# Optimization experiments

Hardware: AMD Instinct MI355X
Metric: run time of the kernel (lower is better)

The kernel has to match this reference:

```python
import jax, jax.numpy as jnp
import numpy as np
from jax.scipy.linalg import expm

N_MODES, N_LAYERS, CUTOFF, BATCH = 6, 6, 3, 1024
M2 = N_MODES * (N_MODES - 1) // 2                  # beamsplitter thetas per interferometer
N_IF = N_MODES * (N_MODES - 1) + (N_MODES - 1)     # interferometer param count = 35

_np_a = np.diag(np.sqrt(np.arange(1, CUTOFF)), 1)  # truncated annihilation operator
A = jnp.asarray(_np_a, jnp.complex64)
AD = A.conj().T
NVEC = jnp.arange(CUTOFF, dtype=jnp.float32)       # number operator diagonal
X_OP = A + AD                                      # x quadrature (hbar=2, PennyLane/SF convention)
BS_GEN = jnp.kron(AD, A) - jnp.kron(A, AD)         # Beamsplitter(theta, 0) generator
SQ_GEN = A @ A - AD @ AD                           # Squeezing(r, 0) generator (times r/2)
D_GEN = AD - A                                     # Displacement(r, 0) generator

def disp_gate(r):
    return expm(r.astype(jnp.complex64) * D_GEN)

def sq_gate(r):
    return expm(0.5 * r.astype(jnp.complex64) * SQ_GEN)

def bs_gate(theta):
    return expm(theta.astype(jnp.complex64) * BS_GEN)

def apply_1(psi, U, m):
    # psi: (B, D, ..., D); apply DxD gate U on mode m
    psi = jnp.moveaxis(psi, 1 + m, -1)
    psi = psi @ U.T
    return jnp.moveaxis(psi, -1, 1 + m)

def apply_1_batched(psi, U, m):
    # U: (B, D, D) per-sample gate (data-encoding displacement)
    psi = jnp.moveaxis(psi, 1 + m, -1)
    psi = jnp.einsum('b...j,bij->b...i', psi, U)
    return jnp.moveaxis(psi, -1, 1 + m)

def apply_2(psi, U, m):
    psi = jnp.moveaxis(psi, (1 + m, 2 + m), (-2, -1))
    sh = psi.shape
    psi = (psi.reshape(sh[:-2] + (CUTOFF * CUTOFF,)) @ U.T).reshape(sh)
    return jnp.moveaxis(psi, (-2, -1), (1 + m, 2 + m))

def apply_diag(psi, d, m):
    shape = [1] * psi.ndim
    shape[1 + m] = CUTOFF
    return psi * d.reshape(shape)

def interferometer(psi, params):
    theta = params[:M2]
    rphi = params[-N_MODES:]  # faithful to source: overlaps last (unused) phi param
    n = 0
    for l in range(N_MODES):
        for k in range(N_MODES - 1):
            if (l + k) % 2 != 1:
                psi = apply_2(psi, bs_gate(theta[n]), k)
                n += 1
    for i in range(max(1, N_MODES - 1)):
        psi = apply_diag(psi, jnp.exp(1j * rphi[i] * NVEC), i)
    return psi

def cv_forward(x, theta_1, theta_2, squeezing_r, displacement_r, kerr_params):
    B = x.shape[0]
    psi = jnp.zeros((B,) + (CUTOFF,) * N_MODES, jnp.complex64)
    psi = psi.at[(slice(None),) + (0,) * N_MODES].set(1.0)  # |0...0> vacuum
    for m in range(N_MODES):  # data-encoding displacements, per-sample gates
        psi = apply_1_batched(psi, jax.vmap(disp_gate)(x[:, m]), m)
    for L in range(N_LAYERS):
        psi = interferometer(psi, theta_1[L])
        for m in range(N_MODES):
            psi = apply_1(psi, sq_gate(squeezing_r[L, m] * 0.5), m)
        psi = interferometer(psi, theta_2[L])
        for m in range(N_MODES):
            psi = apply_1(psi, disp_gate(displacement_r[L, m]), m)
            psi = apply_diag(psi, jnp.exp(1j * (kerr_params[L, m] * 0.001) * NVEC * NVEC), m)
    sum_axes = tuple(range(1, psi.ndim))
    outs = [jnp.sum(jnp.conj(psi) * apply_1(psi, X_OP, m), axis=sum_axes).real
            for m in range(N_MODES)]
    return jnp.stack(outs, axis=1)  # (B, N_MODES)

def setup_inputs() -> dict:
    key = jax.random.key(0)
    ks = jax.random.split(key, 6)
    passive_sd = 0.01 * np.pi
    return {
        'x': jax.random.normal(ks[0], (BATCH, N_MODES), jnp.float32),
        'theta_1': jax.random.normal(ks[1], (N_LAYERS, N_IF), jnp.float32) * passive_sd,
        'theta_2': jax.random.normal(ks[2], (N_LAYERS, N_IF), jnp.float32) * np.float32(0.2 * np.pi),
        'squeezing_r': jax.random.normal(ks[3], (N_LAYERS, N_MODES), jnp.float32) * 1e-3,
        'displacement_r': jax.random.normal(ks[4], (N_LAYERS, N_MODES), jnp.float32) * 1e-3,
        'kerr_params': jax.random.normal(ks[5], (N_LAYERS, N_MODES), jnp.float32) * 1e-3,
    }

def reference(x, theta_1, theta_2, squeezing_r, displacement_r, kerr_params):
    return cv_forward(x, theta_1, theta_2, squeezing_r, displacement_r, kerr_params)
```

## Files before the change

### kernel.cpp

```cpp
#include <hip/hip_runtime.h>

#define SQRT2f 1.41421356237309515f
#define SQRT3f 1.73205080756887729f

__device__ __forceinline__ float2 cmul(float2 a, float2 b) {
  return make_float2(a.x*b.x - a.y*b.y, a.x*b.y + a.y*b.x);
}
__device__ __forceinline__ float2 cadd(float2 a, float2 b) {
  return make_float2(a.x + b.x, a.y + b.y);
}

__device__ __forceinline__ void bs_q(float2 q[9], float2 cs) {
  const float c = cs.x, s = cs.y;
  const float c2 = c*c - s*s, s2 = 2.f*c*s;
  const float cc = c*c, ss = s*s, rcs = SQRT2f*c*s;
  float2 a1=q[1], a3=q[3], a2=q[2], a4=q[4], a6=q[6], a5=q[5], a7=q[7];
  q[1] = make_float2(c*a1.x - s*a3.x, c*a1.y - s*a3.y);
  q[3] = make_float2(s*a1.x + c*a3.x, s*a1.y + c*a3.y);
  q[2] = make_float2(cc*a2.x - rcs*a4.x + ss*a6.x, cc*a2.y - rcs*a4.y + ss*a6.y);
  q[4] = make_float2(rcs*a2.x + c2*a4.x - rcs*a6.x, rcs*a2.y + c2*a4.y - rcs*a6.y);
  q[6] = make_float2(ss*a2.x + rcs*a4.x + cc*a6.x, ss*a2.y + rcs*a4.y + cc*a6.y);
  q[5] = make_float2(c2*a5.x - s2*a7.x, c2*a5.y - s2*a7.y);
  q[7] = make_float2(s2*a5.x + c2*a7.x, s2*a5.y + c2*a7.y);
}

template<int SP>
__device__ __forceinline__ void bs_nonet(float2* __restrict__ psi, int base,
                                         float2 cs) {
  const float c = cs.x, s = cs.y;
  const float c2 = c*c - s*s, s2 = 2.f*c*s;
  const float cc = c*c, ss = s*s, rcs = SQRT2f*c*s;
  float2 a1 = psi[base+SP],   a3 = psi[base+3*SP];
  float2 a2 = psi[base+2*SP], a4 = psi[base+4*SP], a6 = psi[base+6*SP];
  float2 a5 = psi[base+5*SP], a7 = psi[base+7*SP];
  psi[base+SP]   = make_float2(c*a1.x - s*a3.x, c*a1.y - s*a3.y);
  psi[base+3*SP] = make_float2(s*a1.x + c*a3.x, s*a1.y + c*a3.y);
  psi[base+2*SP] = make_float2(cc*a2.x - rcs*a4.x + ss*a6.x,
                               cc*a2.y - rcs*a4.y + ss*a6.y);
  psi[base+4*SP] = make_float2(rcs*a2.x + c2*a4.x - rcs*a6.x,
                               rcs*a2.y + c2*a4.y - rcs*a6.y);
  psi[base+6*SP] = make_float2(ss*a2.x + rcs*a4.x + cc*a6.x,
                               ss*a2.y + rcs*a4.y + cc*a6.y);
  psi[base+5*SP] = make_float2(c2*a5.x - s2*a7.x, c2*a5.y - s2*a7.y);
  psi[base+7*SP] = make_float2(s2*a5.x + c2*a7.x, s2*a5.y + c2*a7.y);
}

template<int SP>
__device__ __forceinline__ void dpbs_nonet(float2* __restrict__ psi, int base,
                                           const float2* __restrict__ G,
                                           float2 cs) {
  const float2* A = G; const float2* B = G + 9;
  float2 v[3][3];
#pragma unroll
  for (int j = 0; j < 3; ++j)
#pragma unroll
    for (int jb = 0; jb < 3; ++jb) v[j][jb] = psi[base + j*3*SP + jb*SP];
  float2 t[3][3];
#pragma unroll
  for (int j = 0; j < 3; ++j)
#pragma unroll
    for (int ib = 0; ib < 3; ++ib)
      t[j][ib] = cadd(cadd(cmul(B[ib*3+0],v[j][0]), cmul(B[ib*3+1],v[j][1])),
                      cmul(B[ib*3+2],v[j][2]));
  float2 q[9];
#pragma unroll
  for (int i = 0; i < 3; ++i)
#pragma unroll
    for (int ib = 0; ib < 3; ++ib)
      q[i*3+ib] = cadd(cadd(cmul(A[i*3+0],t[0][ib]), cmul(A[i*3+1],t[1][ib])),
                       cmul(A[i*3+2],t[2][ib]));
  bs_q(q, cs);
#pragma unroll
  for (int i = 0; i < 3; ++i)
#pragma unroll
    for (int ib = 0; ib < 3; ++ib) psi[base + i*3*SP + ib*SP] = q[i*3+ib];
}

template<int SP>
__device__ __forceinline__ void sqbs_nonet(float2* __restrict__ psi, int base,
                                           const float2* __restrict__ G,
                                           float2 cs) {
  float2 A00=G[0],A02=G[1],A11=G[2],A20=G[3],A22=G[4];
  float2 B00=G[5],B02=G[6],B11=G[7],B20=G[8],B22=G[9];
  float2 v[3][3];
#pragma unroll
  for (int j = 0; j < 3; ++j)
#pragma unroll
    for (int jb = 0; jb < 3; ++jb) v[j][jb] = psi[base + j*3*SP + jb*SP];
  float2 t[3][3];
#pragma unroll
  for (int j = 0; j < 3; ++j) {
    t[j][0] = cadd(cmul(B00,v[j][0]), cmul(B02,v[j][2]));
    t[j][1] = cmul(B11,v[j][1]);
    t[j][2] = cadd(cmul(B20,v[j][0]), cmul(B22,v[j][2]));
  }
  float2 q[9];
#pragma unroll
  for (int ib = 0; ib < 3; ++ib) {
    q[ib]   = cadd(cmul(A00,t[0][ib]), cmul(A02,t[2][ib]));
    q[3+ib] = cmul(A11,t[1][ib]);
    q[6+ib] = cadd(cmul(A20,t[0][ib]), cmul(A22,t[2][ib]));
  }
  bs_q(q, cs);
#pragma unroll
  for (int i = 0; i < 3; ++i)
#pragma unroll
    for (int ib = 0; ib < 3; ++ib) psi[base + i*3*SP + ib*SP] = q[i*3+ib];
}

#define BASE4(g, s0,s1,s2,s3) ({ int _d=(g); int _b=(_d%3)*(s0); _d/=3; \
  _b += (_d%3)*(s1); _d/=3; _b += (_d%3)*(s2); _d/=3; _b += (_d%3)*(s3); _b; })
#define BASE5(g, s0,s1,s2,s3,s4) ({ int _d=(g); int _b=(_d%3)*(s0); _d/=3; \
  _b += (_d%3)*(s1); _d/=3; _b += (_d%3)*(s2); _d/=3; _b += (_d%3)*(s3); _d/=3; \
  _b += (_d%3)*(s4); _b; })

__device__ __forceinline__ float2 dpk_entry(const float* __restrict__ dr,
                                            const float* __restrict__ th2,
                                            const float* __restrict__ kp,
                                            int L, int mode, int i, int j) {
  float sn, cn; sincosf(SQRT3f*dr[L*6+mode], &sn, &cn);
  float sw = sn*(1.f/SQRT3f), cw = (1.f-cn)*(1.f/3.f);
  float U;
  if      (i==0) U = (j==0) ? (1.f-cw)     : (j==1) ? (-sw)         : (SQRT2f*cw);
  else if (i==1) U = (j==0) ? (sw)         : (j==1) ? (1.f-3.f*cw)  : (-SQRT2f*sw);
  else           U = (j==0) ? (SQRT2f*cw)  : (j==1) ? (SQRT2f*sw)   : (1.f-2.f*cw);
  float2 ph = make_float2(1.f, 0.f);
  if (mode < 5) { float ps, pc; sincosf(th2[L*35+29+mode], &ps, &pc);
                  ph = make_float2(pc, ps); }
  float2 phj = (j==0) ? make_float2(1.f,0.f) : (j==1) ? ph : cmul(ph, ph);
  float ks, kc; sincosf(0.001f*kp[L*6+mode], &ks, &kc);
  float2 k1 = make_float2(kc, ks);
  float2 ki = (i==0) ? make_float2(1.f,0.f)
            : (i==1) ? k1 : cmul(cmul(k1,k1), cmul(k1,k1));
  float2 t = cmul(phj, ki);
  return make_float2(U*t.x, U*t.y);
}

__global__ __launch_bounds__(128)
void cvnn_kernel(const float* __restrict__ x,
                 const float* __restrict__ th1,
                 const float* __restrict__ th2,
                 const float* __restrict__ sr,
                 const float* __restrict__ dr,
                 const float* __restrict__ kp,
                 float* __restrict__ out) {
  __shared__ float2 psi[729];
  __shared__ float2 gtab[690];
  __shared__ float red[12];

  const int tid = threadIdx.x;
  const int bidx = blockIdx.x;

  for (int f = tid; f < 690; f += 128) {
    float sn, cn; float2 v;
    if (f < 180) {
      int Lp = f/15, pos = f%15;
      int L = Lp/2, pass = Lp%2;
      float th = (pass ? th2 : th1)[L*35 + pos];
      sincosf(th, &sn, &cn); v = make_float2(cn, sn);
    } else if (f < 360) {
      int i = f - 180; int Lc = i/10, e = i%10;
      int L = Lc/3, c3 = Lc%3;
      int mode = 2*c3 + (e >= 5); int ee = e%5;
      float Sq, Cq; sincosf(0.25f*SQRT2f*sr[L*6+mode], &Sq, &Cq);
      float2 ph = make_float2(1.f, 0.f);
      if (mode < 5) { float ps, pc; sincosf(th1[L*35+29+mode], &ps, &pc);
                      ph = make_float2(pc, ps); }
      float2 ph2 = cmul(ph, ph);
      if      (ee == 0) v = make_float2(Cq, 0.f);
      else if (ee == 1) v = make_float2(Sq*ph2.x, Sq*ph2.y);
      else if (ee == 2) v = ph;
      else if (ee == 3) v = make_float2(-Sq, 0.f);
      else              v = make_float2(Cq*ph2.x, Cq*ph2.y);
    } else if (f < 630) {
      int i = f - 360; int Ld = i/18, e = i%18;
      int Ls = Ld/3, c3 = Ld%3;
      int mode = 2*c3 + (e >= 9); int ee = e%9;
      v = dpk_entry(dr, th2, kp, Ls, mode, ee/3, ee%3);
    } else if (f < 684) {
      int i = f - 630; int m = i/9, e = i%9;
      int ii = e/3, jj = e%3;
      float2 D0i = dpk_entry(dr, th2, kp, 5, m, 0, ii);
      float2 D1i = dpk_entry(dr, th2, kp, 5, m, 1, ii);
      float2 D2i = dpk_entry(dr, th2, kp, 5, m, 2, ii);
      float2 D0j = dpk_entry(dr, th2, kp, 5, m, 0, jj);
      float2 D1j = dpk_entry(dr, th2, kp, 5, m, 1, jj);
      float2 D2j = dpk_entry(dr, th2, kp, 5, m, 2, jj);
      float2 c0 = make_float2(D0i.x, -D0i.y);
      float2 c1 = make_float2(D1i.x, -D1i.y);
      float2 c2 = make_float2(D2i.x, -D2i.y);
      float2 acc = cmul(c0, D1j);
      float2 tmp = make_float2(D0j.x + SQRT2f*D2j.x, D0j.y + SQRT2f*D2j.y);
      acc = cadd(acc, cmul(c1, tmp));
      acc = cadd(acc, cmul(c2, make_float2(SQRT2f*D1j.x, SQRT2f*D1j.y)));
      v = acc;
    } else {
      int mode = f - 684;
      sincosf(SQRT3f*x[bidx*6 + mode], &sn, &cn);
      v = make_float2(sn*(1.f/SQRT3f), (1.f-cn)*(1.f/3.f));
    }
    gtab[f] = v;
  }
  __syncthreads();

  for (int idx = tid; idx < 729; idx += 128) {
    float pr = 1.f; int d = idx;
#pragma unroll
    for (int mm = 5; mm >= 0; --mm) {
      int n = d % 3; d /= 3;
      float2 dc = gtab[684 + mm];
      pr *= (n==0) ? (1.f-dc.y) : (n==1) ? dc.x : SQRT2f*dc.y;
    }
    psi[idx] = make_float2(pr, 0.f);
  }

  const bool act = (tid < 81);
  const int g = (tid < 81) ? tid : 0;
  const int b0 = g;
  const int b1 = BASE4(g, 1, 3, 9, 243);
  const int b2 = BASE4(g, 1, 3, 81, 243);
  const int b3 = BASE4(g, 1, 27, 81, 243);
  const int b4 = BASE4(g, 9, 27, 81, 243);
  __syncthreads();

  float2 csN = gtab[0];
  __syncthreads();

#define BSP(SP, BB, NEXT)  { if (act) bs_nonet<SP>(psi, BB, csN); \
    csN = gtab[NEXT]; __syncthreads(); }
#define DPBS(SP, BB, GI, NEXT) { if (act) dpbs_nonet<SP>(psi, BB, &gtab[GI], csN); \
    csN = gtab[NEXT]; __syncthreads(); }
#define SQBS(SP, BB, GI, NEXT) { if (act) sqbs_nonet<SP>(psi, BB, &gtab[GI], csN); \
    csN = gtab[NEXT]; __syncthreads(); }

#pragma unroll
  for (int L = 0; L < 6; ++L) {
    const int i1 = (L*2)*15, i2 = (L*2+1)*15;
    if (L == 0) {
      BSP(81, b0, i1+1); BSP(9, b2, i1+2); BSP(1, b4, i1+3);
    } else {
      const int gd = 360 + (L-1)*3*18;
      DPBS(81, b0, gd+0,  i1+1); DPBS(9, b2, gd+18, i1+2); DPBS(1, b4, gd+36, i1+3);
    }
    BSP(27, b1, i1+4);  BSP(3, b3, i1+5);
    BSP(81, b0, i1+6);  BSP(9, b2, i1+7);  BSP(1, b4, i1+8);
    BSP(27, b1, i1+9);  BSP(3, b3, i1+10);
    BSP(81, b0, i1+11); BSP(9, b2, i1+12); BSP(1, b4, i1+13);
    BSP(27, b1, i1+14); BSP(3, b3, i2+0);
    {
      const int gs = 180 + L*3*10;
      SQBS(81, b0, gs+0, i2+1); SQBS(9, b2, gs+10, i2+2); SQBS(1, b4, gs+20, i2+3);
    }
    BSP(27, b1, i2+4);  BSP(3, b3, i2+5);
    BSP(81, b0, i2+6);  BSP(9, b2, i2+7);  BSP(1, b4, i2+8);
    BSP(27, b1, i2+9);  BSP(3, b3, i2+10);
    BSP(81, b0, i2+11); BSP(9, b2, i2+12); BSP(1, b4, i2+13);
    BSP(27, b1, i2+14); BSP(3, b3, (L < 5) ? (L+1)*30 : 0);
  }

  float xs[6] = {0.f, 0.f, 0.f, 0.f, 0.f, 0.f};
  for (int it = 0; it < 2; ++it) {
    int t = tid + (it << 7);
    if (t < 243) {
#define XACC(m, SS, BB) { int b_ = (BB); \
      float2 a_ = psi[b_]; float2 e_ = psi[b_+(SS)]; float2 f_ = psi[b_+2*(SS)]; \
      const float2* M_ = &gtab[630 + (m)*9]; \
      float d0 = M_[0].x, d1 = M_[4].x, d2 = M_[8].x; \
      float2 M01 = M_[1], M02 = M_[2], M12 = M_[5]; \
      xs[m] += d0*(a_.x*a_.x + a_.y*a_.y) + d1*(e_.x*e_.x + e_.y*e_.y) \
             + d2*(f_.x*f_.x + f_.y*f_.y) \
        + 2.f*(M01.x*(a_.x*e_.x + a_.y*e_.y) - M01.y*(a_.x*e_.y - a_.y*e_.x)) \
        + 2.f*(M02.x*(a_.x*f_.x + a_.y*f_.y) - M02.y*(a_.x*f_.y - a_.y*f_.x)) \
        + 2.f*(M12.x*(e_.x*f_.x + e_.y*f_.y) - M12.y*(e_.x*f_.y - e_.y*f_.x)); }
      XACC(0, 243, BASE5(t, 1, 3, 9, 27, 81));
      XACC(1, 81,  BASE5(t, 1, 3, 9, 27, 243));
      XACC(2, 27,  BASE5(t, 1, 3, 9, 81, 243));
      XACC(3, 9,   BASE5(t, 1, 3, 27, 81, 243));
      XACC(4, 3,   BASE5(t, 1, 9, 27, 81, 243));
      XACC(5, 1,   BASE5(t, 3, 9, 27, 81, 243));
    }
  }
  const int lane = tid & 63, wid = tid >> 6;
#pragma unroll
  for (int m = 0; m < 6; ++m) {
    float v = xs[m];
    for (int off = 32; off > 0; off >>= 1) v += __shfl_down(v, off);
    if (lane == 0) red[wid*6 + m] = v;
  }
  __syncthreads();
  if (tid < 6) out[bidx*6 + tid] = red[tid] + red[6 + tid];
}

extern "C" void kernel_launch(void* const* d_in, const int* in_sizes, int n_in,
                              void* d_out, int out_size, void* d_ws, size_t ws_size,
                              hipStream_t stream) {
  const float* x  = (const float*)d_in[0];
  const float* t1 = (const float*)d_in[1];
  const float* t2 = (const float*)d_in[2];
  const float* sr = (const float*)d_in[3];
  const float* dr = (const float*)d_in[4];
  const float* kp = (const float*)d_in[5];
  const int B = in_sizes[0] / 6;
  cvnn_kernel<<<B, 128, 0, stream>>>(x, t1, t2, sr, dr, kp, (float*)d_out);
}
```

Baseline: 92.86 us.

## Pad last mode to 4 and process two-amplitude float4 groups per thread

```diff
diff --git a/kernel.cpp b/kernel.cpp
--- a/kernel.cpp
+++ b/kernel.cpp
@@ -10,102 +10,184 @@
   return make_float2(a.x + b.x, a.y + b.y);
 }
 
-__device__ __forceinline__ void bs_q(float2 q[9], float2 cs) {
-  const float c = cs.x, s = cs.y;
-  const float c2 = c*c - s*s, s2 = 2.f*c*s;
-  const float cc = c*c, ss = s*s, rcs = SQRT2f*c*s;
-  float2 a1=q[1], a3=q[3], a2=q[2], a4=q[4], a6=q[6], a5=q[5], a7=q[7];
-  q[1] = make_float2(c*a1.x - s*a3.x, c*a1.y - s*a3.y);
-  q[3] = make_float2(s*a1.x + c*a3.x, s*a1.y + c*a3.y);
-  q[2] = make_float2(cc*a2.x - rcs*a4.x + ss*a6.x, cc*a2.y - rcs*a4.y + ss*a6.y);
-  q[4] = make_float2(rcs*a2.x + c2*a4.x - rcs*a6.x, rcs*a2.y + c2*a4.y - rcs*a6.y);
-  q[6] = make_float2(ss*a2.x + rcs*a4.x + cc*a6.x, ss*a2.y + rcs*a4.y + cc*a6.y);
-  q[5] = make_float2(c2*a5.x - s2*a7.x, c2*a5.y - s2*a7.y);
-  q[7] = make_float2(s2*a5.x + c2*a7.x, s2*a5.y + c2*a7.y);
-}
-
-template<int SP>
-__device__ __forceinline__ void bs_nonet(float2* __restrict__ psi, int base,
-                                         float2 cs) {
-  const float c = cs.x, s = cs.y;
-  const float c2 = c*c - s*s, s2 = 2.f*c*s;
-  const float cc = c*c, ss = s*s, rcs = SQRT2f*c*s;
-  float2 a1 = psi[base+SP],   a3 = psi[base+3*SP];
-  float2 a2 = psi[base+2*SP], a4 = psi[base+4*SP], a6 = psi[base+6*SP];
-  float2 a5 = psi[base+5*SP], a7 = psi[base+7*SP];
-  psi[base+SP]   = make_float2(c*a1.x - s*a3.x, c*a1.y - s*a3.y);
-  psi[base+3*SP] = make_float2(s*a1.x + c*a3.x, s*a1.y + c*a3.y);
-  psi[base+2*SP] = make_float2(cc*a2.x - rcs*a4.x + ss*a6.x,
-                               cc*a2.y - rcs*a4.y + ss*a6.y);
-  psi[base+4*SP] = make_float2(rcs*a2.x + c2*a4.x - rcs*a6.x,
-                               rcs*a2.y + c2*a4.y - rcs*a6.y);
-  psi[base+6*SP] = make_float2(ss*a2.x + rcs*a4.x + cc*a6.x,
-                               ss*a2.y + rcs*a4.y + cc*a6.y);
-  psi[base+5*SP] = make_float2(c2*a5.x - s2*a7.x, c2*a5.y - s2*a7.y);
-  psi[base+7*SP] = make_float2(s2*a5.x + c2*a7.x, s2*a5.y + c2*a7.y);
-}
-
-template<int SP>
-__device__ __forceinline__ void dpbs_nonet(float2* __restrict__ psi, int base,
-                                           const float2* __restrict__ G,
-                                           float2 cs) {
-  const float2* A = G; const float2* B = G + 9;
-  float2 v[3][3];
-#pragma unroll
-  for (int j = 0; j < 3; ++j)
-#pragma unroll
-    for (int jb = 0; jb < 3; ++jb) v[j][jb] = psi[base + j*3*SP + jb*SP];
-  float2 t[3][3];
-#pragma unroll
-  for (int j = 0; j < 3; ++j)
-#pragma unroll
-    for (int ib = 0; ib < 3; ++ib)
-      t[j][ib] = cadd(cadd(cmul(B[ib*3+0],v[j][0]), cmul(B[ib*3+1],v[j][1])),
-                      cmul(B[ib*3+2],v[j][2]));
-  float2 q[9];
-#pragma unroll
-  for (int i = 0; i < 3; ++i)
-#pragma unroll
-    for (int ib = 0; ib < 3; ++ib)
-      q[i*3+ib] = cadd(cadd(cmul(A[i*3+0],t[0][ib]), cmul(A[i*3+1],t[1][ib])),
-                       cmul(A[i*3+2],t[2][ib]));
-  bs_q(q, cs);
-#pragma unroll
-  for (int i = 0; i < 3; ++i)
-#pragma unroll
-    for (int ib = 0; ib < 3; ++ib) psi[base + i*3*SP + ib*SP] = q[i*3+ib];
-}
-
-template<int SP>
-__device__ __forceinline__ void sqbs_nonet(float2* __restrict__ psi, int base,
-                                           const float2* __restrict__ G,
-                                           float2 cs) {
+__device__ __forceinline__ float4 f4m(float a, float4 v) {
+  return make_float4(a*v.x, a*v.y, a*v.z, a*v.w);
+}
+__device__ __forceinline__ float4 f4ma(float a, float4 v, float4 acc) {
+  return make_float4(acc.x+a*v.x, acc.y+a*v.y, acc.z+a*v.z, acc.w+a*v.w);
+}
+__device__ __forceinline__ float4 f4ms(float a, float4 v, float4 acc) {
+  return make_float4(acc.x-a*v.x, acc.y-a*v.y, acc.z-a*v.z, acc.w-a*v.w);
+}
+__device__ __forceinline__ float4 cmul4(float2 C, float4 v) {
+  return make_float4(C.x*v.x - C.y*v.y, C.x*v.y + C.y*v.x,
+                     C.x*v.z - C.y*v.w, C.x*v.w + C.y*v.z);
+}
+__device__ __forceinline__ float4 cfma4(float2 C, float4 v, float4 acc) {
+  return make_float4(acc.x + C.x*v.x - C.y*v.y, acc.y + C.x*v.y + C.y*v.x,
+                     acc.z + C.x*v.z - C.y*v.w, acc.w + C.x*v.w + C.y*v.z);
+}
+
+#define BS4C(v01,v02,v10,v11,v12,v20,v21, c,s,c2,s2,cc,ss,rcs) { \
+  { float4 t1=v01, t3=v10; \
+    v01 = f4ms(s,t3,f4m(c,t1)); v10 = f4ma(c,t3,f4m(s,t1)); } \
+  { float4 t2=v02, t4=v11, t6=v20; \
+    v02 = f4ma(ss,t6, f4ms(rcs,t4, f4m(cc,t2))); \
+    v11 = f4ms(rcs,t6, f4ma(c2,t4, f4m(rcs,t2))); \
+    v20 = f4ma(cc,t6, f4ma(rcs,t4, f4m(ss,t2))); } \
+  { float4 t5=v12, t7=v21; \
+    v12 = f4ms(s2,t7, f4m(c2,t5)); v21 = f4ma(c2,t7, f4m(s2,t5)); } }
+
+template<int SO, int SI>
+__device__ __forceinline__ void bs_w(float4* __restrict__ P, int b, float2 cs) {
+  const float c=cs.x, s=cs.y;
+  const float c2=c*c-s*s, s2=2.f*c*s, cc=c*c, ss=s*s, rcs=SQRT2f*c*s;
+  float4 v01=P[b+SI],      v10=P[b+SO];
+  float4 v02=P[b+2*SI],    v11=P[b+SO+SI],  v20=P[b+2*SO];
+  float4 v12=P[b+SO+2*SI], v21=P[b+2*SO+SI];
+  BS4C(v01,v02,v10,v11,v12,v20,v21, c,s,c2,s2,cc,ss,rcs);
+  P[b+SI]=v01; P[b+SO]=v10; P[b+2*SI]=v02; P[b+SO+SI]=v11; P[b+2*SO]=v20;
+  P[b+SO+2*SI]=v12; P[b+2*SO+SI]=v21;
+}
+
+template<int SO, int SI>
+__device__ __forceinline__ void sqbs_w(float4* __restrict__ P, int b,
+                                       const float2* __restrict__ G, float2 cs) {
   float2 A00=G[0],A02=G[1],A11=G[2],A20=G[3],A22=G[4];
   float2 B00=G[5],B02=G[6],B11=G[7],B20=G[8],B22=G[9];
-  float2 v[3][3];
-#pragma unroll
-  for (int j = 0; j < 3; ++j)
-#pragma unroll
-    for (int jb = 0; jb < 3; ++jb) v[j][jb] = psi[base + j*3*SP + jb*SP];
-  float2 t[3][3];
-#pragma unroll
-  for (int j = 0; j < 3; ++j) {
-    t[j][0] = cadd(cmul(B00,v[j][0]), cmul(B02,v[j][2]));
-    t[j][1] = cmul(B11,v[j][1]);
-    t[j][2] = cadd(cmul(B20,v[j][0]), cmul(B22,v[j][2]));
-  }
-  float2 q[9];
-#pragma unroll
-  for (int ib = 0; ib < 3; ++ib) {
-    q[ib]   = cadd(cmul(A00,t[0][ib]), cmul(A02,t[2][ib]));
-    q[3+ib] = cmul(A11,t[1][ib]);
-    q[6+ib] = cadd(cmul(A20,t[0][ib]), cmul(A22,t[2][ib]));
-  }
-  bs_q(q, cs);
-#pragma unroll
-  for (int i = 0; i < 3; ++i)
-#pragma unroll
-    for (int ib = 0; ib < 3; ++ib) psi[base + i*3*SP + ib*SP] = q[i*3+ib];
+  float4 v00=P[b],      v01=P[b+SI],      v02=P[b+2*SI];
+  float4 v10=P[b+SO],   v11=P[b+SO+SI],   v12=P[b+SO+2*SI];
+  float4 v20=P[b+2*SO], v21=P[b+2*SO+SI], v22=P[b+2*SO+2*SI];
+  { float4 u0=v00,u2=v02; v00=cfma4(B02,u2,cmul4(B00,u0)); v01=cmul4(B11,v01); v02=cfma4(B22,u2,cmul4(B20,u0)); }
+  { float4 u0=v10,u2=v12; v10=cfma4(B02,u2,cmul4(B00,u0)); v11=cmul4(B11,v11); v12=cfma4(B22,u2,cmul4(B20,u0)); }
+  { float4 u0=v20,u2=v22; v20=cfma4(B02,u2,cmul4(B00,u0)); v21=cmul4(B11,v21); v22=cfma4(B22,u2,cmul4(B20,u0)); }
+  { float4 u0=v00,u2=v20; v00=cfma4(A02,u2,cmul4(A00,u0)); v10=cmul4(A11,v10); v20=cfma4(A22,u2,cmul4(A20,u0)); }
+  { float4 u0=v01,u2=v21; v01=cfma4(A02,u2,cmul4(A00,u0)); v11=cmul4(A11,v11); v21=cfma4(A22,u2,cmul4(A20,u0)); }
+  { float4 u0=v02,u2=v22; v02=cfma4(A02,u2,cmul4(A00,u0)); v12=cmul4(A11,v12); v22=cfma4(A22,u2,cmul4(A20,u0)); }
+  const float c=cs.x, s=cs.y;
+  const float c2=c*c-s*s, s2=2.f*c*s, cc=c*c, ss=s*s, rcs=SQRT2f*c*s;
+  BS4C(v01,v02,v10,v11,v12,v20,v21, c,s,c2,s2,cc,ss,rcs);
+  P[b]=v00; P[b+SI]=v01; P[b+2*SI]=v02;
+  P[b+SO]=v10; P[b+SO+SI]=v11; P[b+SO+2*SI]=v12;
+  P[b+2*SO]=v20; P[b+2*SO+SI]=v21; P[b+2*SO+2*SI]=v22;
+}
+
+template<int SO, int SI>
+__device__ __forceinline__ void dpbs_w(float4* __restrict__ P, int b,
+                                       const float2* __restrict__ G, float2 cs) {
+  float4 v00=P[b],      v01=P[b+SI],      v02=P[b+2*SI];
+  float4 v10=P[b+SO],   v11=P[b+SO+SI],   v12=P[b+SO+2*SI];
+  float4 v20=P[b+2*SO], v21=P[b+2*SO+SI], v22=P[b+2*SO+2*SI];
+  { float4 u0=v00,u1=v01,u2=v02;
+    v00 = cfma4(G[11],u2, cfma4(G[10],u1, cmul4(G[9], u0)));
+    v01 = cfma4(G[14],u2, cfma4(G[13],u1, cmul4(G[12],u0)));
+    v02 = cfma4(G[17],u2, cfma4(G[16],u1, cmul4(G[15],u0))); }
+  { float4 u0=v10,u1=v11,u2=v12;
+    v10 = cfma4(G[11],u2, cfma4(G[10],u1, cmul4(G[9], u0)));
+    v11 = cfma4(G[14],u2, cfma4(G[13],u1, cmul4(G[12],u0)));
+    v12 = cfma4(G[17],u2, cfma4(G[16],u1, cmul4(G[15],u0))); }
+  { float4 u0=v20,u1=v21,u2=v22;
+    v20 = cfma4(G[11],u2, cfma4(G[10],u1, cmul4(G[9], u0)));
+    v21 = cfma4(G[14],u2, cfma4(G[13],u1, cmul4(G[12],u0)));
+    v22 = cfma4(G[17],u2, cfma4(G[16],u1, cmul4(G[15],u0))); }
+  { float4 u0=v00,u1=v10,u2=v20;
+    v00 = cfma4(G[2],u2, cfma4(G[1],u1, cmul4(G[0],u0)));
+    v10 = cfma4(G[5],u2, cfma4(G[4],u1, cmul4(G[3],u0)));
+    v20 = cfma4(G[8],u2, cfma4(G[7],u1, cmul4(G[6],u0))); }
+  { float4 u0=v01,u1=v11,u2=v21;
+    v01 = cfma4(G[2],u2, cfma4(G[1],u1, cmul4(G[0],u0)));
+    v11 = cfma4(G[5],u2, cfma4(G[4],u1, cmul4(G[3],u0)));
+    v21 = cfma4(G[8],u2, cfma4(G[7],u1, cmul4(G[6],u0))); }
+  { float4 u0=v02,u1=v12,u2=v22;
+    v02 = cfma4(G[2],u2, cfma4(G[1],u1, cmul4(G[0],u0)));
+    v12 = cfma4(G[5],u2, cfma4(G[4],u1, cmul4(G[3],u0)));
+    v22 = cfma4(G[8],u2, cfma4(G[7],u1, cmul4(G[6],u0))); }
+  const float c=cs.x, s=cs.y;
+  const float c2=c*c-s*s, s2=2.f*c*s, cc=c*c, ss=s*s, rcs=SQRT2f*c*s;
+  BS4C(v01,v02,v10,v11,v12,v20,v21, c,s,c2,s2,cc,ss,rcs);
+  P[b]=v00; P[b+SI]=v01; P[b+2*SI]=v02;
+  P[b+SO]=v10; P[b+SO+SI]=v11; P[b+SO+2*SI]=v12;
+  P[b+2*SO]=v20; P[b+2*SO+SI]=v21; P[b+2*SO+2*SI]=v22;
+}
+
+#define BS2C(v01,v02,v10,v11,v12,v20,v21, c,s,c2,s2,cc,ss,rcs) { \
+  { float2 t1=v01, t3=v10; \
+    v01 = make_float2(c*t1.x - s*t3.x, c*t1.y - s*t3.y); \
+    v10 = make_float2(s*t1.x + c*t3.x, s*t1.y + c*t3.y); } \
+  { float2 t2=v02, t4=v11, t6=v20; \
+    v02 = make_float2(cc*t2.x - rcs*t4.x + ss*t6.x, cc*t2.y - rcs*t4.y + ss*t6.y); \
+    v11 = make_float2(rcs*t2.x + c2*t4.x - rcs*t6.x, rcs*t2.y + c2*t4.y - rcs*t6.y); \
+    v20 = make_float2(ss*t2.x + rcs*t4.x + cc*t6.x, ss*t2.y + rcs*t4.y + cc*t6.y); } \
+  { float2 t5=v12, t7=v21; \
+    v12 = make_float2(c2*t5.x - s2*t7.x, c2*t5.y - s2*t7.y); \
+    v21 = make_float2(s2*t5.x + c2*t7.x, s2*t5.y + c2*t7.y); } }
+
+__device__ __forceinline__ void bs_n4(float2* __restrict__ p2, int b, float2 cs) {
+  const float c=cs.x, s=cs.y;
+  const float c2=c*c-s*s, s2=2.f*c*s, cc=c*c, ss=s*s, rcs=SQRT2f*c*s;
+  float2 v01=p2[b+1], v02=p2[b+2], v10=p2[b+4], v11=p2[b+5], v12=p2[b+6];
+  float2 v20=p2[b+8], v21=p2[b+9];
+  BS2C(v01,v02,v10,v11,v12,v20,v21, c,s,c2,s2,cc,ss,rcs);
+  p2[b+1]=v01; p2[b+2]=v02; p2[b+4]=v10; p2[b+5]=v11; p2[b+6]=v12;
+  p2[b+8]=v20; p2[b+9]=v21;
+}
+
+__device__ __forceinline__ void sqbs_n4(float2* __restrict__ p2, int b,
+                                        const float2* __restrict__ G, float2 cs) {
+  float2 A00=G[0],A02=G[1],A11=G[2],A20=G[3],A22=G[4];
+  float2 B00=G[5],B02=G[6],B11=G[7],B20=G[8],B22=G[9];
+  float2 v00=p2[b],   v01=p2[b+1], v02=p2[b+2];
+  float2 v10=p2[b+4], v11=p2[b+5], v12=p2[b+6];
+  float2 v20=p2[b+8], v21=p2[b+9], v22=p2[b+10];
+  { float2 u0=v00,u2=v02; v00=cadd(cmul(B00,u0),cmul(B02,u2)); v01=cmul(B11,v01); v02=cadd(cmul(B20,u0),cmul(B22,u2)); }
+  { float2 u0=v10,u2=v12; v10=cadd(cmul(B00,u0),cmul(B02,u2)); v11=cmul(B11,v11); v12=cadd(cmul(B20,u0),cmul(B22,u2)); }
+  { float2 u0=v20,u2=v22; v20=cadd(cmul(B00,u0),cmul(B02,u2)); v21=cmul(B11,v21); v22=cadd(cmul(B20,u0),cmul(B22,u2)); }
+  { float2 u0=v00,u2=v20; v00=cadd(cmul(A00,u0),cmul(A02,u2)); v10=cmul(A11,v10); v20=cadd(cmul(A20,u0),cmul(A22,u2)); }
+  { float2 u0=v01,u2=v21; v01=cadd(cmul(A00,u0),cmul(A02,u2)); v11=cmul(A11,v11); v21=cadd(cmul(A20,u0),cmul(A22,u2)); }
+  { float2 u0=v02,u2=v22; v02=cadd(cmul(A00,u0),cmul(A02,u2)); v12=cmul(A11,v12); v22=cadd(cmul(A20,u0),cmul(A22,u2)); }
+  const float c=cs.x, s=cs.y;
+  const float c2=c*c-s*s, s2=2.f*c*s, cc=c*c, ss=s*s, rcs=SQRT2f*c*s;
+  BS2C(v01,v02,v10,v11,v12,v20,v21, c,s,c2,s2,cc,ss,rcs);
+  p2[b]=v00;   p2[b+1]=v01; p2[b+2]=v02;
+  p2[b+4]=v10; p2[b+5]=v11; p2[b+6]=v12;
+  p2[b+8]=v20; p2[b+9]=v21; p2[b+10]=v22;
+}
+
+__device__ __forceinline__ void dpbs_n4(float2* __restrict__ p2, int b,
+                                        const float2* __restrict__ G, float2 cs) {
+  float2 v00=p2[b],   v01=p2[b+1], v02=p2[b+2];
+  float2 v10=p2[b+4], v11=p2[b+5], v12=p2[b+6];
+  float2 v20=p2[b+8], v21=p2[b+9], v22=p2[b+10];
+  { float2 u0=v00,u1=v01,u2=v02;
+    v00=cadd(cadd(cmul(G[9],u0),cmul(G[10],u1)),cmul(G[11],u2));
+    v01=cadd(cadd(cmul(G[12],u0),cmul(G[13],u1)),cmul(G[14],u2));
+    v02=cadd(cadd(cmul(G[15],u0),cmul(G[16],u1)),cmul(G[17],u2)); }
+  { float2 u0=v10,u1=v11,u2=v12;
+    v10=cadd(cadd(cmul(G[9],u0),cmul(G[10],u1)),cmul(G[11],u2));
+    v11=cadd(cadd(cmul(G[12],u0),cmul(G[13],u1)),cmul(G[14],u2));
+    v12=cadd(cadd(cmul(G[15],u0),cmul(G[16],u1)),cmul(G[17],u2)); }
+  { float2 u0=v20,u1=v21,u2=v22;
+    v20=cadd(cadd(cmul(G[9],u0),cmul(G[10],u1)),cmul(G[11],u2));
+    v21=cadd(cadd(cmul(G[12],u0),cmul(G[13],u1)),cmul(G[14],u2));
+    v22=cadd(cadd(cmul(G[15],u0),cmul(G[16],u1)),cmul(G[17],u2)); }
+  { float2 u0=v00,u1=v10,u2=v20;
+    v00=cadd(cadd(cmul(G[0],u0),cmul(G[1],u1)),cmul(G[2],u2));
+    v10=cadd(cadd(cmul(G[3],u0),cmul(G[4],u1)),cmul(G[5],u2));
+    v20=cadd(cadd(cmul(G[6],u0),cmul(G[7],u1)),cmul(G[8],u2)); }
+  { float2 u0=v01,u1=v11,u2=v21;
+    v01=cadd(cadd(cmul(G[0],u0),cmul(G[1],u1)),cmul(G[2],u2));
+    v11=cadd(cadd(cmul(G[3],u0),cmul(G[4],u1)),cmul(G[5],u2));
+    v21=cadd(cadd(cmul(G[6],u0),cmul(G[7],u1)),cmul(G[8],u2)); }
+  { float2 u0=v02,u1=v12,u2=v22;
+    v02=cadd(cadd(cmul(G[0],u0),cmul(G[1],u1)),cmul(G[2],u2));
+    v12=cadd(cadd(cmul(G[3],u0),cmul(G[4],u1)),cmul(G[5],u2));
+    v22=cadd(cadd(cmul(G[6],u0),cmul(G[7],u1)),cmul(G[8],u2)); }
+  const float c=cs.x, s=cs.y;
+  const float c2=c*c-s*s, s2=2.f*c*s, cc=c*c, ss=s*s, rcs=SQRT2f*c*s;
+  BS2C(v01,v02,v10,v11,v12,v20,v21, c,s,c2,s2,cc,ss,rcs);
+  p2[b]=v00;   p2[b+1]=v01; p2[b+2]=v02;
+  p2[b+4]=v10; p2[b+5]=v11; p2[b+6]=v12;
+  p2[b+8]=v20; p2[b+9]=v21; p2[b+10]=v22;
 }
 
 #define BASE4(g, s0,s1,s2,s3) ({ int _d=(g); int _b=(_d%3)*(s0); _d/=3; \
@@ -144,9 +226,11 @@
                  const float* __restrict__ dr,
                  const float* __restrict__ kp,
                  float* __restrict__ out) {
-  __shared__ float2 psi[729];
+  __shared__ float4 psi4[486];
   __shared__ float2 gtab[690];
   __shared__ float red[12];
+  float2* psi2 = (float2*)psi4;
+  float4* P4 = psi4;
 
   const int tid = threadIdx.x;
   const int bidx = blockIdx.x;
@@ -203,89 +287,113 @@
   }
   __syncthreads();
 
-  for (int idx = tid; idx < 729; idx += 128) {
-    float pr = 1.f; int d = idx;
+  for (int idx = tid; idx < 972; idx += 128) {
+    int n5 = idx & 3;
+    float pr = 0.f;
+    if (n5 != 3) {
+      float2 d5 = gtab[684 + 5];
+      pr = (n5==0) ? (1.f-d5.y) : (n5==1) ? d5.x : SQRT2f*d5.y;
+      int d = idx >> 2;
 #pragma unroll
-    for (int mm = 5; mm >= 0; --mm) {
-      int n = d % 3; d /= 3;
-      float2 dc = gtab[684 + mm];
-      pr *= (n==0) ? (1.f-dc.y) : (n==1) ? dc.x : SQRT2f*dc.y;
+      for (int mm = 4; mm >= 0; --mm) {
+        int n = d % 3; d /= 3;
+        float2 dc = gtab[684 + mm];
+        pr *= (n==0) ? (1.f-dc.y) : (n==1) ? dc.x : SQRT2f*dc.y;
+      }
     }
-    psi[idx] = make_float2(pr, 0.f);
+    psi2[idx] = make_float2(pr, 0.f);
   }
 
-  const bool act = (tid < 81);
-  const int g = (tid < 81) ? tid : 0;
-  const int b0 = g;
-  const int b1 = BASE4(g, 1, 3, 9, 243);
-  const int b2 = BASE4(g, 1, 3, 81, 243);
-  const int b3 = BASE4(g, 1, 27, 81, 243);
-  const int b4 = BASE4(g, 9, 27, 81, 243);
+  const int p  = tid & 1;
+  const int cw = (tid < 54) ? (tid >> 1) : 0;
+  const int wx = cw/9, wy = (cw/3)%3, wz = cw%3;
+  const int bw0 = wx*18  + wy*6  + wz*2  + p;
+  const int bw1 = wx*162 + wy*6  + wz*2  + p;
+  const int bw2 = wx*162 + wy*54 + wz*2  + p;
+  const int bw3 = wx*162 + wy*54 + wz*18 + p;
+  const int g4 = (tid < 81) ? tid : 0;
+  const int b4n = BASE4(g4, 12, 36, 108, 324);
   __syncthreads();
 
   float2 csN = gtab[0];
   __syncthreads();
 
-#define BSP(SP, BB, NEXT)  { if (act) bs_nonet<SP>(psi, BB, csN); \
-    csN = gtab[NEXT]; __syncthreads(); }
-#define DPBS(SP, BB, GI, NEXT) { if (act) dpbs_nonet<SP>(psi, BB, &gtab[GI], csN); \
-    csN = gtab[NEXT]; __syncthreads(); }
-#define SQBS(SP, BB, GI, NEXT) { if (act) sqbs_nonet<SP>(psi, BB, &gtab[GI], csN); \
+#define BSW0(NEXT) { if (tid < 54) bs_w<162,54>(P4, bw0, csN); \
+    csN = gtab[NEXT]; __syncthreads(); }
+#define BSW1(NEXT) { if (tid < 54) bs_w<54,18>(P4, bw1, csN); \
+    csN = gtab[NEXT]; __syncthreads(); }
+#define BSW2(NEXT) { if (tid < 54) bs_w<18,6>(P4, bw2, csN); \
+    csN = gtab[NEXT]; __syncthreads(); }
+#define BSW3(NEXT) { if (tid < 54) bs_w<6,2>(P4, bw3, csN); \
+    csN = gtab[NEXT]; __syncthreads(); }
+#define BSN4(NEXT) { if (tid < 81) bs_n4(psi2, b4n, csN); \
+    csN = gtab[NEXT]; __syncthreads(); }
+#define SQW0(GS,NEXT) { if (tid < 54) sqbs_w<162,54>(P4, bw0, &gtab[GS], csN); \
+    csN = gtab[NEXT]; __syncthreads(); }
+#define SQW2(GS,NEXT) { if (tid < 54) sqbs_w<18,6>(P4, bw2, &gtab[GS], csN); \
+    csN = gtab[NEXT]; __syncthreads(); }
+#define SQN4(GS,NEXT) { if (tid < 81) sqbs_n4(psi2, b4n, &gtab[GS], csN); \
+    csN = gtab[NEXT]; __syncthreads(); }
+#define DPW0(GD,NEXT) { if (tid < 54) dpbs_w<162,54>(P4, bw0, &gtab[GD], csN); \
+    csN = gtab[NEXT]; __syncthreads(); }
+#define DPW2(GD,NEXT) { if (tid < 54) dpbs_w<18,6>(P4, bw2, &gtab[GD], csN); \
+    csN = gtab[NEXT]; __syncthreads(); }
+#define DPN4(GD,NEXT) { if (tid < 81) dpbs_n4(psi2, b4n, &gtab[GD], csN); \
     csN = gtab[NEXT]; __syncthreads(); }
 
 #pragma unroll
   for (int L = 0; L < 6; ++L) {
     const int i1 = (L*2)*15, i2 = (L*2+1)*15;
     if (L == 0) {
-      BSP(81, b0, i1+1); BSP(9, b2, i1+2); BSP(1, b4, i1+3);
+      BSW0(i1+1); BSW2(i1+2); BSN4(i1+3);
     } else {
-      const int gd = 360 + (L-1)*3*18;
-      DPBS(81, b0, gd+0,  i1+1); DPBS(9, b2, gd+18, i1+2); DPBS(1, b4, gd+36, i1+3);
+      const int gd = 360 + (L-1)*54;
+      DPW0(gd+0, i1+1); DPW2(gd+18, i1+2); DPN4(gd+36, i1+3);
     }
-    BSP(27, b1, i1+4);  BSP(3, b3, i1+5);
-    BSP(81, b0, i1+6);  BSP(9, b2, i1+7);  BSP(1, b4, i1+8);
-    BSP(27, b1, i1+9);  BSP(3, b3, i1+10);
-    BSP(81, b0, i1+11); BSP(9, b2, i1+12); BSP(1, b4, i1+13);
-    BSP(27, b1, i1+14); BSP(3, b3, i2+0);
+    BSW1(i1+4);  BSW3(i1+5);
+    BSW0(i1+6);  BSW2(i1+7);  BSN4(i1+8);
+    BSW1(i1+9);  BSW3(i1+10);
+    BSW0(i1+11); BSW2(i1+12); BSN4(i1+13);
+    BSW1(i1+14); BSW3(i2+0);
     {
-      const int gs = 180 + L*3*10;
-      SQBS(81, b0, gs+0, i2+1); SQBS(9, b2, gs+10, i2+2); SQBS(1, b4, gs+20, i2+3);
+      const int gs = 180 + L*30;
+      SQW0(gs+0, i2+1); SQW2(gs+10, i2+2); SQN4(gs+20, i2+3);
     }
-    BSP(27, b1, i2+4);  BSP(3, b3, i2+5);
-    BSP(81, b0, i2+6);  BSP(9, b2, i2+7);  BSP(1, b4, i2+8);
-    BSP(27, b1, i2+9);  BSP(3, b3, i2+10);
-    BSP(81, b0, i2+11); BSP(9, b2, i2+12); BSP(1, b4, i2+13);
-    BSP(27, b1, i2+14); BSP(3, b3, (L < 5) ? (L+1)*30 : 0);
+    BSW1(i2+4);  BSW3(i2+5);
+    BSW0(i2+6);  BSW2(i2+7);  BSN4(i2+8);
+    BSW1(i2+9);  BSW3(i2+10);
+    BSW0(i2+11); BSW2(i2+12); BSN4(i2+13);
+    BSW1(i2+14); BSW3((L < 5) ? (L+1)*30 : 0);
   }
 
-  float xs[6] = {0.f, 0.f, 0.f, 0.f, 0.f, 0.f};
+  float xs[6] = {0.f,0.f,0.f,0.f,0.f,0.f};
   for (int it = 0; it < 2; ++it) {
     int t = tid + (it << 7);
     if (t < 243) {
 #define XACC(m, SS, BB) { int b_ = (BB); \
-      float2 a_ = psi[b_]; float2 e_ = psi[b_+(SS)]; float2 f_ = psi[b_+2*(SS)]; \
       const float2* M_ = &gtab[630 + (m)*9]; \
       float d0 = M_[0].x, d1 = M_[4].x, d2 = M_[8].x; \
       float2 M01 = M_[1], M02 = M_[2], M12 = M_[5]; \
+      float2 a_ = psi2[b_]; float2 e_ = psi2[b_+(SS)]; float2 f_ = psi2[b_+2*(SS)]; \
       xs[m] += d0*(a_.x*a_.x + a_.y*a_.y) + d1*(e_.x*e_.x + e_.y*e_.y) \
              + d2*(f_.x*f_.x + f_.y*f_.y) \
         + 2.f*(M01.x*(a_.x*e_.x + a_.y*e_.y) - M01.y*(a_.x*e_.y - a_.y*e_.x)) \
         + 2.f*(M02.x*(a_.x*f_.x + a_.y*f_.y) - M02.y*(a_.x*f_.y - a_.y*f_.x)) \
         + 2.f*(M12.x*(e_.x*f_.x + e_.y*f_.y) - M12.y*(e_.x*f_.y - e_.y*f_.x)); }
-      XACC(0, 243, BASE5(t, 1, 3, 9, 27, 81));
-      XACC(1, 81,  BASE5(t, 1, 3, 9, 27, 243));
-      XACC(2, 27,  BASE5(t, 1, 3, 9, 81, 243));
-      XACC(3, 9,   BASE5(t, 1, 3, 27, 81, 243));
-      XACC(4, 3,   BASE5(t, 1, 9, 27, 81, 243));
-      XACC(5, 1,   BASE5(t, 3, 9, 27, 81, 243));
+      XACC(0, 324, BASE5(t, 1, 4, 12, 36, 108));
+      XACC(1, 108, BASE5(t, 1, 4, 12, 36, 324));
+      XACC(2, 36,  BASE5(t, 1, 4, 12, 108, 324));
+      XACC(3, 12,  BASE5(t, 1, 4, 36, 108, 324));
+      XACC(4, 4,   BASE5(t, 1, 12, 36, 108, 324));
+      XACC(5, 1,   BASE5(t, 4, 12, 36, 108, 324));
     }
   }
-  const int lane = tid & 63, wid = tid >> 6;
+  const int wid = tid >> 6;
 #pragma unroll
   for (int m = 0; m < 6; ++m) {
     float v = xs[m];
     for (int off = 32; off > 0; off >>= 1) v += __shfl_down(v, off);
-    if (lane == 0) red[wid*6 + m] = v;
+    if ((tid & 63) == 0) red[wid*6 + m] = v;
   }
   __syncthreads();
   if (tid < 6) out[bidx*6 + tid] = red[tid] + red[6 + tid];
```

Result: slower. 99.05 us (+6.7%).
